# Optimization experiments

Hardware: AMD Instinct MI355X
Metric: run time of the kernel (lower is better)

The kernel has to match this reference:

```python
import jax, jax.numpy as jnp
import numpy as np

B, T, D, C = 8, 4096, 768, 2048

def setup_inputs() -> dict:
    key = jax.random.key(0)
    k1, k2 = jax.random.split(key)
    embed = jax.random.normal(k1, (B, T, D), dtype=jnp.float32)
    cluster_centers = jax.random.normal(k2, (C, D), dtype=jnp.float32)
    return {"embed": embed, "cluster_centers": cluster_centers}

def reference(embed, cluster_centers):
    x_sq = jnp.sum(embed * embed, axis=-1, keepdims=True)          # (b, t, 1)
    c_sq = jnp.sum(cluster_centers * cluster_centers, axis=-1)     # (c,)
    cross = jnp.einsum('btd,cd->btc', embed, cluster_centers)      # (b, t, c)
    sq_dists = x_sq + c_sq[None, None, :] - 2.0 * cross
    dists = jnp.sqrt(jnp.maximum(sq_dists, 0.0))
    # dists argmax of -cdist == argmin of cdist
    clusters = jnp.argmin(dists, axis=-1)                          # (b, t) int
    return clusters
```

## Files before the change

### kernel.cpp

```cpp
#include <hip/hip_runtime.h>

typedef __fp16 f16x2 __attribute__((ext_vector_type(2)));
typedef __fp16 f16x8 __attribute__((ext_vector_type(8)));
typedef float f32x4 __attribute__((ext_vector_type(4)));

constexpr int MM = 32768;
constexpr int NN = 2048;
constexpr int KK = 768;
constexpr int NKT = KK / 32;
constexpr int NA_UNITS = (MM / 16) * NKT;
constexpr int NB_UNITS = (NN / 16) * NKT;

constexpr size_t WS_APACK = 0;
constexpr size_t WS_BPACK = WS_APACK + (size_t)MM * KK * 4;
constexpr size_t WS_CSQ   = WS_BPACK + (size_t)NN * KK * 4;
constexpr size_t WS_SLOT  = WS_CSQ + (size_t)NN * 4;
constexpr size_t WS_NEED  = WS_SLOT + (size_t)MM * 16 * 8;

__device__ __forceinline__ unsigned bc(f16x2 h) {
    return __builtin_bit_cast(unsigned, h);
}


__global__ __launch_bounds__(256)
void fragpack_kernel(const float* __restrict__ A, const float* __restrict__ Bc,
                     uint4* __restrict__ Ap, uint4* __restrict__ Bp,
                     float* __restrict__ csq) {
    const int task = blockIdx.x * 4 + (threadIdx.x >> 6);
    const int lane = threadIdx.x & 63;

    if (task >= NA_UNITS + NB_UNITS) {
        const int cl = task - (NA_UNITS + NB_UNITS);
        const float4* row = reinterpret_cast<const float4*>(Bc + (size_t)cl * KK);
        float s = 0.f;
#pragma unroll
        for (int w = 0; w < KK / (4 * 64); ++w) {
            float4 v = row[w * 64 + lane];
            s = fmaf(v.x, v.x, s); s = fmaf(v.y, v.y, s);
            s = fmaf(v.z, v.z, s); s = fmaf(v.w, v.w, s);
        }
#pragma unroll
        for (int off = 32; off > 0; off >>= 1) s += __shfl_xor(s, off, 64);
        if (lane == 0) csq[cl] = s;
        return;
    }

    const int ln15 = lane & 15;
    const int quad = lane >> 4;

    const bool isB = task >= NA_UNITS;
    const int t = isB ? task - NA_UNITS : task;
    const int tile = t / NKT, kt = t % NKT;
    const float* src = (isB ? Bc : A) + (size_t)(tile * 16 + ln15) * KK + kt * 32 + quad * 8;
    uint4* dst = (isB ? Bp : Ap) + (size_t)t * 128 + lane;

    const float4 v0 = *(const float4*)(src);
    const float4 v1 = *(const float4*)(src + 4);
    f16x2 h0 = __builtin_amdgcn_cvt_pkrtz(v0.x, v0.y);
    f16x2 h1 = __builtin_amdgcn_cvt_pkrtz(v0.z, v0.w);
    f16x2 h2 = __builtin_amdgcn_cvt_pkrtz(v1.x, v1.y);
    f16x2 h3 = __builtin_amdgcn_cvt_pkrtz(v1.z, v1.w);
    f16x2 l0 = __builtin_amdgcn_cvt_pkrtz(v0.x-(float)h0[0], v0.y-(float)h0[1]);
    f16x2 l1 = __builtin_amdgcn_cvt_pkrtz(v0.z-(float)h1[0], v0.w-(float)h1[1]);
    f16x2 l2 = __builtin_amdgcn_cvt_pkrtz(v1.x-(float)h2[0], v1.y-(float)h2[1]);
    f16x2 l3 = __builtin_amdgcn_cvt_pkrtz(v1.z-(float)h3[0], v1.w-(float)h3[1]);
    uint4 hv = {bc(h0), bc(h1), bc(h2), bc(h3)};
    uint4 lv = {bc(l0), bc(l1), bc(l2), bc(l3)};
    dst[0]  = hv;
    dst[64] = lv;
}

__global__ __launch_bounds__(64)
void csq_kernel(const float* __restrict__ cc, float* __restrict__ csq) {
    const int cl = blockIdx.x;
    const int lane = threadIdx.x;
    const float4* row = reinterpret_cast<const float4*>(cc + (size_t)cl * KK);
    float s = 0.f;
#pragma unroll
    for (int w = 0; w < KK / (4 * 64); ++w) {
        float4 v = row[w * 64 + lane];
        s = fmaf(v.x, v.x, s); s = fmaf(v.y, v.y, s);
        s = fmaf(v.z, v.z, s); s = fmaf(v.w, v.w, s);
    }
#pragma unroll
    for (int off = 32; off > 0; off >>= 1) s += __shfl_xor(s, off, 64);
    if (lane == 0) csq[cl] = s;
}

#define MF2(a, b, c) __builtin_amdgcn_mfma_f32_16x16x32_f16(a, b, c, 0, 0, 0)
#define DSB() __builtin_amdgcn_sched_barrier(0)

__global__ __launch_bounds__(256, 3)
void gemm_pack_kernel(const uint4* __restrict__ Ap, const uint4* __restrict__ Bp,
                      const float* __restrict__ csq, uint2* __restrict__ slots) {
    __shared__ uint4 ldsq[2048];

    const int b   = blockIdx.x;
    const int xcd = b & 7;
    const int s   = b >> 3;
    const int gx  = s & 15;
    const int gy  = xcd + ((s >> 4) << 3);

    const int tid  = threadIdx.x;
    const int lane = tid & 63;
    const int ln15 = lane & 15;
    const int quad = lane >> 4;
    const int wave = tid >> 6;
    const int wm   = wave >> 1;
    const int wn   = wave & 1;
    const int tbase = gy * 128;
    const int cb    = gx * 128;

    const uint4* sp[8];
#pragma unroll
    for (int q = 0; q < 8; ++q) {
        const int u = wave * 8 + q;
        const bool isA = u < 16;
        const int v = isA ? u : u - 16;
        const int tile = (isA ? gy * 8 : gx * 8) + (v >> 1);
        const int part = v & 1;
        sp[q] = (isA ? Ap : Bp) + (size_t)tile * NKT * 128 + part * 64 + lane;
    }

#define STAGE_ALL(kt_) { if ((kt_) < NKT) {                                   \
    _Pragma("unroll")                                                         \
    for (int qq = 0; qq < 8; ++qq)                                            \
        __builtin_amdgcn_global_load_lds(                                     \
            (const __attribute__((address_space(1))) unsigned int*)(sp[qq] + (kt_) * 128), \
            (__attribute__((address_space(3))) unsigned int*)&ldsq[(wave * 8 + qq) * 64], \
            16, 0, 0); } }

    f32x4 acc[4][4];
#pragma unroll
    for (int i = 0; i < 4; ++i)
#pragma unroll
        for (int j = 0; j < 4; ++j) { f32x4 z = {0.f,0.f,0.f,0.f}; acc[i][j] = z; }

    f16x8 Bh[4], Bl[4], Ah[4], Al[4];

#define RD_ALL() {                                                            \
    _Pragma("unroll")                                                         \
    for (int j = 0; j < 4; ++j) {                                             \
        const int nu = 16 + (wn * 4 + j) * 2;                                 \
        Bh[j] = *(const f16x8*)&ldsq[nu * 64 + lane];                         \
        Bl[j] = *(const f16x8*)&ldsq[(nu + 1) * 64 + lane];                   \
    }                                                                         \
    _Pragma("unroll")                                                         \
    for (int i = 0; i < 4; ++i) {                                             \
        const int au = (wm * 4 + i) * 2;                                      \
        Ah[i] = *(const f16x8*)&ldsq[au * 64 + lane];                         \
        Al[i] = *(const f16x8*)&ldsq[(au + 1) * 64 + lane];                   \
    } }

#define MFMA_I2(i_) {                                                         \
    _Pragma("unroll")                                                         \
    for (int j = 0; j < 4; ++j) acc[i_][j] = MF2(Ah[i_], Bh[j], acc[i_][j]);  \
    _Pragma("unroll")                                                         \
    for (int j = 0; j < 4; ++j) acc[i_][j] = MF2(Ah[i_], Bl[j], acc[i_][j]);  \
    _Pragma("unroll")                                                         \
    for (int j = 0; j < 4; ++j) acc[i_][j] = MF2(Al[i_], Bh[j], acc[i_][j]);  \
}

#define WAIT_VM0()   { asm volatile("s_waitcnt vmcnt(0)" ::: "memory"); DSB(); }
#define WAIT_LGKM0() { asm volatile("s_waitcnt lgkmcnt(0)" ::: "memory"); DSB(); }
#define BARRIER()    { DSB(); __builtin_amdgcn_s_barrier(); DSB(); }

    STAGE_ALL(0)
    WAIT_VM0(); BARRIER();

#pragma unroll 1
    for (int kt = 0; kt < NKT; ++kt) {
        RD_ALL()
        MFMA_I2(0)
        WAIT_LGKM0();
        BARRIER();
        STAGE_ALL(kt + 1)
        DSB();
        MFMA_I2(1)
        MFMA_I2(2)
        MFMA_I2(3)
        WAIT_VM0();
        BARRIER();
    }

    float csq4[4];
#pragma unroll
    for (int j = 0; j < 4; ++j) csq4[j] = csq[cb + wn * 64 + j * 16 + ln15];

    float bval[16]; int bidx[16];
#pragma unroll
    for (int i = 0; i < 4; ++i)
#pragma unroll
        for (int r = 0; r < 4; ++r) {
            const int rid = i * 4 + r;
            float bv_ = csq4[0] - 2.0f * acc[i][0][r];
            int   bi_ = cb + wn * 64 + ln15;
#pragma unroll
            for (int j = 1; j < 4; ++j) {
                const float s2 = csq4[j] - 2.0f * acc[i][j][r];
                const int   c = cb + wn * 64 + j * 16 + ln15;
                if (s2 < bv_) { bv_ = s2; bi_ = c; }
            }
            bval[rid] = bv_; bidx[rid] = bi_;
        }
#pragma unroll
    for (int off = 1; off < 16; off <<= 1) {
#pragma unroll
        for (int rid = 0; rid < 16; ++rid) {
            const float ov = __shfl_xor(bval[rid], off, 64);
            const int   oi = __shfl_xor(bidx[rid], off, 64);
            if (ov < bval[rid] || (ov == bval[rid] && oi < bidx[rid])) {
                bval[rid] = ov; bidx[rid] = oi;
            }
        }
    }

    __syncthreads();
    float* vtab = (float*)&ldsq[0];
    int*   itab = (int*)&ldsq[64];
    if (ln15 == 0) {
#pragma unroll
        for (int i = 0; i < 4; ++i)
#pragma unroll
            for (int r = 0; r < 4; ++r) {
                const int row = wm * 64 + i * 16 + quad * 4 + r;
                vtab[row * 2 + wn] = bval[i * 4 + r];
                itab[row * 2 + wn] = bidx[i * 4 + r];
            }
    }
    __syncthreads();
    if (tid < 128) {
        float v0 = vtab[tid * 2]; int i0 = itab[tid * 2];
        const float v1 = vtab[tid * 2 + 1]; const int i1 = itab[tid * 2 + 1];
        if (v1 < v0 || (v1 == v0 && i1 < i0)) { v0 = v1; i0 = i1; }
        uint2 e; e.x = __float_as_uint(v0); e.y = (unsigned)i0;
        slots[(size_t)(tbase + tid) * 16 + gx] = e;
    }
}

__global__ __launch_bounds__(256)
void slot_reduce_kernel(const uint2* __restrict__ slots, int* __restrict__ out) {
    const int t = blockIdx.x * 256 + threadIdx.x;
    const uint2* s = slots + (size_t)t * 16;
    float bv = __uint_as_float(s[0].x); int bi = (int)s[0].y;
#pragma unroll
    for (int j = 1; j < 16; ++j) {
        const uint2 e = s[j];
        const float v = __uint_as_float(e.x);
        if (v < bv || (v == bv && (int)e.y < bi)) { bv = v; bi = (int)e.y; }
    }
    out[t] = bi;
}


__global__ __launch_bounds__(256)
void init_ws_kernel(unsigned long long* __restrict__ w) {
    w[blockIdx.x * 256 + threadIdx.x] = 0xFFFFFFFFFFFFFFFFull;
}

__global__ __launch_bounds__(256, 2)
void argmin_mfma_kernel(const float* __restrict__ A, const float* __restrict__ Bc,
                        const float* __restrict__ csq,
                        unsigned long long* __restrict__ ws64) {
    __shared__ unsigned lds[4 * 128 * 20];
    constexpr int AH = 0, AL = 2560, BH = 5120;

    const int tid  = threadIdx.x;
    const int lane = tid & 63;
    const int ln15 = lane & 15;
    const int quad = lane >> 4;
    const int wave = tid >> 6;
    const int wm = wave >> 1, wn = wave & 1;
    const int tbase = blockIdx.x * 128;
    const int cb    = blockIdx.y * 128;

    const int sr  = tid >> 1;
    const int skh = tid & 1;
    const float* gA = A  + (size_t)(tbase + sr) * KK + skh * 16;
    const float* gB = Bc + (size_t)(cb   + sr) * KK + skh * 16;
    const int wword = sr * 20 + skh * 8;

    f32x4 acc[4][4];
#pragma unroll
    for (int i = 0; i < 4; ++i)
#pragma unroll
        for (int j = 0; j < 4; ++j) { f32x4 z = {0.f,0.f,0.f,0.f}; acc[i][j] = z; }

    float4 av[4], bv[4];
#pragma unroll
    for (int p = 0; p < 4; ++p) {
        av[p] = *(const float4*)(gA + p * 4);
        bv[p] = *(const float4*)(gB + p * 4);
    }

    int aw[4], bw[4];
#pragma unroll
    for (int i = 0; i < 4; ++i) {
        aw[i] = AH + (wm * 64 + i * 16 + ln15) * 20 + quad * 4;
        bw[i] = BH + (wn * 64 + i * 16 + ln15) * 20 + quad * 4;
    }

    for (int k0 = 0; k0 < KK; k0 += 32) {
        __syncthreads();
#pragma unroll
        for (int h = 0; h < 2; ++h) {
            float4 v0 = av[2*h], v1 = av[2*h+1];
            f16x2 h00 = __builtin_amdgcn_cvt_pkrtz(v0.x, v0.y);
            f16x2 h01 = __builtin_amdgcn_cvt_pkrtz(v0.z, v0.w);
            f16x2 h10 = __builtin_amdgcn_cvt_pkrtz(v1.x, v1.y);
            f16x2 h11 = __builtin_amdgcn_cvt_pkrtz(v1.z, v1.w);
            f16x2 l00 = __builtin_amdgcn_cvt_pkrtz(v0.x-(float)h00[0], v0.y-(float)h00[1]);
            f16x2 l01 = __builtin_amdgcn_cvt_pkrtz(v0.z-(float)h01[0], v0.w-(float)h01[1]);
            f16x2 l10 = __builtin_amdgcn_cvt_pkrtz(v1.x-(float)h10[0], v1.y-(float)h10[1]);
            f16x2 l11 = __builtin_amdgcn_cvt_pkrtz(v1.z-(float)h11[0], v1.w-(float)h11[1]);
            uint4 hv = {bc(h00), bc(h01), bc(h10), bc(h11)};
            uint4 lv = {bc(l00), bc(l01), bc(l10), bc(l11)};
            *(uint4*)&lds[AH + wword + 4*h] = hv;
            *(uint4*)&lds[AL + wword + 4*h] = lv;

            float4 w0 = bv[2*h], w1 = bv[2*h+1];
            f16x2 g00 = __builtin_amdgcn_cvt_pkrtz(w0.x, w0.y);
            f16x2 g01 = __builtin_amdgcn_cvt_pkrtz(w0.z, w0.w);
            f16x2 g10 = __builtin_amdgcn_cvt_pkrtz(w1.x, w1.y);
            f16x2 g11 = __builtin_amdgcn_cvt_pkrtz(w1.z, w1.w);
            f16x2 m00 = __builtin_amdgcn_cvt_pkrtz(w0.x-(float)g00[0], w0.y-(float)g00[1]);
            f16x2 m01 = __builtin_amdgcn_cvt_pkrtz(w0.z-(float)g01[0], w0.w-(float)g01[1]);
            f16x2 m10 = __builtin_amdgcn_cvt_pkrtz(w1.x-(float)g10[0], w1.y-(float)g10[1]);
            f16x2 m11 = __builtin_amdgcn_cvt_pkrtz(w1.z-(float)g11[0], w1.w-(float)g11[1]);
            uint4 gv = {bc(g00), bc(g01), bc(g10), bc(g11)};
            uint4 mv = {bc(m00), bc(m01), bc(m10), bc(m11)};
            *(uint4*)&lds[BH + wword + 4*h]        = gv;
            *(uint4*)&lds[BH + 2560 + wword + 4*h] = mv;
        }
        __syncthreads();

        const int kn = k0 + 32;
        if (kn < KK) {
#pragma unroll
            for (int p = 0; p < 4; ++p) {
                av[p] = *(const float4*)(gA + kn + p * 4);
                bv[p] = *(const float4*)(gB + kn + p * 4);
            }
        }

        f16x8 a_h[4], a_l[4], b_h[4], b_l[4];
#pragma unroll
        for (int i = 0; i < 4; ++i) {
            a_h[i] = *(const f16x8*)&lds[aw[i]];
            a_l[i] = *(const f16x8*)&lds[aw[i] + 2560];
            b_h[i] = *(const f16x8*)&lds[bw[i]];
            b_l[i] = *(const f16x8*)&lds[bw[i] + 2560];
        }
#pragma unroll
        for (int i = 0; i < 4; ++i)
#pragma unroll
            for (int j = 0; j < 4; ++j) {
                acc[i][j] = __builtin_amdgcn_mfma_f32_16x16x32_f16(a_h[i], b_h[j], acc[i][j], 0, 0, 0);
                acc[i][j] = __builtin_amdgcn_mfma_f32_16x16x32_f16(a_h[i], b_l[j], acc[i][j], 0, 0, 0);
                acc[i][j] = __builtin_amdgcn_mfma_f32_16x16x32_f16(a_l[i], b_h[j], acc[i][j], 0, 0, 0);
            }
    }

    float csq4[4];
#pragma unroll
    for (int j = 0; j < 4; ++j) csq4[j] = csq[cb + wn * 64 + j * 16 + ln15];

    float bval[16]; int bidx[16];
#pragma unroll
    for (int i = 0; i < 4; ++i)
#pragma unroll
        for (int r = 0; r < 4; ++r) {
            const int rid = i * 4 + r;
            float bv_ = csq4[0] - 2.0f * acc[i][0][r];
            int   bi_ = cb + wn * 64 + ln15;
#pragma unroll
            for (int j = 1; j < 4; ++j) {
                const float s = csq4[j] - 2.0f * acc[i][j][r];
                const int   c = cb + wn * 64 + j * 16 + ln15;
                if (s < bv_) { bv_ = s; bi_ = c; }
            }
            bval[rid] = bv_; bidx[rid] = bi_;
        }
#pragma unroll
    for (int off = 1; off < 16; off <<= 1) {
#pragma unroll
        for (int rid = 0; rid < 16; ++rid) {
            const float ov = __shfl_xor(bval[rid], off, 64);
            const int   oi = __shfl_xor(bidx[rid], off, 64);
            if (ov < bval[rid] || (ov == bval[rid] && oi < bidx[rid])) {
                bval[rid] = ov; bidx[rid] = oi;
            }
        }
    }

    __syncthreads();
    float* vtab = (float*)&lds[0];
    int*   itab = (int*)&lds[256];
    if (ln15 == 0) {
#pragma unroll
        for (int i = 0; i < 4; ++i)
#pragma unroll
            for (int r = 0; r < 4; ++r) {
                const int row = wm * 64 + i * 16 + quad * 4 + r;
                vtab[row * 2 + wn] = bval[i * 4 + r];
                itab[row * 2 + wn] = bidx[i * 4 + r];
            }
    }
    __syncthreads();
    if (tid < 128) {
        float v0 = vtab[tid * 2]; int i0 = itab[tid * 2];
        const float v1 = vtab[tid * 2 + 1]; const int i1 = itab[tid * 2 + 1];
        if (v1 < v0 || (v1 == v0 && i1 < i0)) { v0 = v1; i0 = i1; }
        const unsigned b   = __float_as_uint(v0);
        const unsigned key = (b & 0x80000000u) ? ~b : (b | 0x80000000u);
        const unsigned long long pk =
            ((unsigned long long)key << 32) | (unsigned long long)(unsigned)i0;
        atomicMin(&ws64[tbase + tid], pk);
    }
}

__global__ __launch_bounds__(256)
void unpack_kernel(const unsigned long long* __restrict__ w, int* __restrict__ out) {
    const int i = blockIdx.x * 256 + threadIdx.x;
    out[i] = (int)(unsigned)(w[i] & 0xFFFFFFFFull);
}

extern "C" void kernel_launch(void* const* d_in, const int* in_sizes, int n_in,
                              void* d_out, int out_size, void* d_ws, size_t ws_size,
                              hipStream_t stream) {
    const float* embed   = (const float*)d_in[0];
    const float* centers = (const float*)d_in[1];
    int* out = (int*)d_out;

    if (ws_size >= WS_NEED) {
        uint4* Ap = (uint4*)((char*)d_ws + WS_APACK);
        uint4* Bp = (uint4*)((char*)d_ws + WS_BPACK);
        float* csq   = (float*)((char*)d_ws + WS_CSQ);
        uint2* slots = (uint2*)((char*)d_ws + WS_SLOT);
        fragpack_kernel<<<(NA_UNITS + NB_UNITS + NN) / 4, 256, 0, stream>>>(
            embed, centers, Ap, Bp, csq);
        gemm_pack_kernel<<<(MM / 128) * (NN / 128), 256, 0, stream>>>(
            Ap, Bp, csq, slots);
        slot_reduce_kernel<<<MM / 256, 256, 0, stream>>>(slots, out);
    } else {
        unsigned long long* ws64 = (unsigned long long*)d_ws;
        float* csq = (float*)((char*)d_ws + (size_t)MM * 8);
        init_ws_kernel<<<MM / 256, 256, 0, stream>>>(ws64);
        csq_kernel<<<NN, 64, 0, stream>>>(centers, csq);
        argmin_mfma_kernel<<<dim3(MM / 128, NN / 128), 256, 0, stream>>>(
            embed, centers, csq, ws64);
        unpack_kernel<<<MM / 256, 256, 0, stream>>>(ws64, out);
    }
}
```

Baseline: 435.4 us.

## Switch split-fp16 GEMM from 16x16x32 to 32x32x16 MFMA tiles

Repacks A and B fragments into 32-row by 16-k units and rewrites the GEMM inner loop to use 32x32x16 f16 MFMA with 2x2 accumulator tiles per wave instead of 4x4 16x16 tiles. The larger MFMA cuts the instruction count and LDS fragment reads per k-step. The argmin epilogue is rewritten for the 32x32 accumulator layout, with a 5-step shuffle reduction across 32 lanes. This risks different register pressure and epilogue shuffle cost.

```diff
diff --git a/kernel.cpp b/kernel.cpp
--- a/kernel.cpp
+++ b/kernel.cpp
@@ -3,13 +3,15 @@
 typedef __fp16 f16x2 __attribute__((ext_vector_type(2)));
 typedef __fp16 f16x8 __attribute__((ext_vector_type(8)));
 typedef float f32x4 __attribute__((ext_vector_type(4)));
+typedef float f32x16 __attribute__((ext_vector_type(16)));
 
 constexpr int MM = 32768;
 constexpr int NN = 2048;
 constexpr int KK = 768;
 constexpr int NKT = KK / 32;
-constexpr int NA_UNITS = (MM / 16) * NKT;
-constexpr int NB_UNITS = (NN / 16) * NKT;
+constexpr int NKT16 = KK / 16;
+constexpr int NA_UNITS = (MM / 32) * NKT16;
+constexpr int NB_UNITS = (NN / 32) * NKT16;
 
 constexpr size_t WS_APACK = 0;
 constexpr size_t WS_BPACK = WS_APACK + (size_t)MM * KK * 4;
@@ -45,13 +47,13 @@
         return;
     }
 
-    const int ln15 = lane & 15;
-    const int quad = lane >> 4;
+    const int ln31 = lane & 31;
+    const int half = lane >> 5;
 
     const bool isB = task >= NA_UNITS;
     const int t = isB ? task - NA_UNITS : task;
-    const int tile = t / NKT, kt = t % NKT;
-    const float* src = (isB ? Bc : A) + (size_t)(tile * 16 + ln15) * KK + kt * 32 + quad * 8;
+    const int tile = t / NKT16, kt = t % NKT16;
+    const float* src = (isB ? Bc : A) + (size_t)(tile * 32 + ln31) * KK + kt * 16 + half * 8;
     uint4* dst = (isB ? Bp : Ap) + (size_t)t * 128 + lane;
 
     const float4 v0 = *(const float4*)(src);
@@ -87,7 +89,7 @@
     if (lane == 0) csq[cl] = s;
 }
 
-#define MF2(a, b, c) __builtin_amdgcn_mfma_f32_16x16x32_f16(a, b, c, 0, 0, 0)
+#define MF32(a, b, c) __builtin_amdgcn_mfma_f32_32x32x16_f16(a, b, c, 0, 0, 0)
 #define DSB() __builtin_amdgcn_sched_barrier(0)
 
 __global__ __launch_bounds__(256, 3)
@@ -103,8 +105,8 @@
 
     const int tid  = threadIdx.x;
     const int lane = tid & 63;
-    const int ln15 = lane & 15;
-    const int quad = lane >> 4;
+    const int ln31 = lane & 31;
+    const int hi   = lane >> 5;
     const int wave = tid >> 6;
     const int wm   = wave >> 1;
     const int wn   = wave & 1;
@@ -116,49 +118,67 @@
     for (int q = 0; q < 8; ++q) {
         const int u = wave * 8 + q;
         const bool isA = u < 16;
-        const int v = isA ? u : u - 16;
-        const int tile = (isA ? gy * 8 : gx * 8) + (v >> 1);
+        const int v = u & 15;
+        const int tile = (isA ? gy * 4 : gx * 4) + (v >> 2);
+        const int ksub = (v >> 1) & 1;
         const int part = v & 1;
-        sp[q] = (isA ? Ap : Bp) + (size_t)tile * NKT * 128 + part * 64 + lane;
+        sp[q] = (isA ? Ap : Bp) + (size_t)(tile * NKT16 + ksub) * 128 + part * 64 + lane;
     }
 
 #define STAGE_ALL(kt_) { if ((kt_) < NKT) {                                   \
     _Pragma("unroll")                                                         \
     for (int qq = 0; qq < 8; ++qq)                                            \
         __builtin_amdgcn_global_load_lds(                                     \
-            (const __attribute__((address_space(1))) unsigned int*)(sp[qq] + (kt_) * 128), \
+            (const __attribute__((address_space(1))) unsigned int*)(sp[qq] + (kt_) * 256), \
             (__attribute__((address_space(3))) unsigned int*)&ldsq[(wave * 8 + qq) * 64], \
             16, 0, 0); } }
 
-    f32x4 acc[4][4];
-#pragma unroll
-    for (int i = 0; i < 4; ++i)
-#pragma unroll
-        for (int j = 0; j < 4; ++j) { f32x4 z = {0.f,0.f,0.f,0.f}; acc[i][j] = z; }
-
-    f16x8 Bh[4], Bl[4], Ah[4], Al[4];
+    f32x16 acc[2][2];
+#pragma unroll
+    for (int i = 0; i < 2; ++i)
+#pragma unroll
+        for (int j = 0; j < 2; ++j)
+#pragma unroll
+            for (int r = 0; r < 16; ++r) acc[i][j][r] = 0.f;
+
+    f16x8 Ah[2][2], Al[2][2], Bh[2][2], Bl[2][2];
 
 #define RD_ALL() {                                                            \
     _Pragma("unroll")                                                         \
-    for (int j = 0; j < 4; ++j) {                                             \
-        const int nu = 16 + (wn * 4 + j) * 2;                                 \
-        Bh[j] = *(const f16x8*)&ldsq[nu * 64 + lane];                         \
-        Bl[j] = *(const f16x8*)&ldsq[(nu + 1) * 64 + lane];                   \
+    for (int nj = 0; nj < 2; ++nj) {                                          \
+        const int nt = wn * 2 + nj;                                           \
+        _Pragma("unroll")                                                     \
+        for (int ks = 0; ks < 2; ++ks) {                                      \
+            Bh[nj][ks] = *(const f16x8*)&ldsq[1024 + (nt * 4 + ks * 2) * 64 + lane];     \
+            Bl[nj][ks] = *(const f16x8*)&ldsq[1024 + (nt * 4 + ks * 2 + 1) * 64 + lane]; \
+        }                                                                     \
     }                                                                         \
     _Pragma("unroll")                                                         \
-    for (int i = 0; i < 4; ++i) {                                             \
-        const int au = (wm * 4 + i) * 2;                                      \
-        Ah[i] = *(const f16x8*)&ldsq[au * 64 + lane];                         \
-        Al[i] = *(const f16x8*)&ldsq[(au + 1) * 64 + lane];                   \
+    for (int mi = 0; mi < 2; ++mi) {                                          \
+        const int mt = wm * 2 + mi;                                           \
+        _Pragma("unroll")                                                     \
+        for (int ks = 0; ks < 2; ++ks) {                                      \
+            Ah[mi][ks] = *(const f16x8*)&ldsq[(mt * 4 + ks * 2) * 64 + lane];            \
+            Al[mi][ks] = *(const f16x8*)&ldsq[(mt * 4 + ks * 2 + 1) * 64 + lane];        \
+        }                                                                     \
     } }
 
-#define MFMA_I2(i_) {                                                         \
-    _Pragma("unroll")                                                         \
-    for (int j = 0; j < 4; ++j) acc[i_][j] = MF2(Ah[i_], Bh[j], acc[i_][j]);  \
-    _Pragma("unroll")                                                         \
-    for (int j = 0; j < 4; ++j) acc[i_][j] = MF2(Ah[i_], Bl[j], acc[i_][j]);  \
-    _Pragma("unroll")                                                         \
-    for (int j = 0; j < 4; ++j) acc[i_][j] = MF2(Al[i_], Bh[j], acc[i_][j]);  \
+#define MFMA_KS(ks_) {                                                        \
+    _Pragma("unroll")                                                         \
+    for (int mi = 0; mi < 2; ++mi)                                            \
+        _Pragma("unroll")                                                     \
+        for (int nj = 0; nj < 2; ++nj)                                        \
+            acc[mi][nj] = MF32(Ah[mi][ks_], Bh[nj][ks_], acc[mi][nj]);        \
+    _Pragma("unroll")                                                         \
+    for (int mi = 0; mi < 2; ++mi)                                            \
+        _Pragma("unroll")                                                     \
+        for (int nj = 0; nj < 2; ++nj)                                        \
+            acc[mi][nj] = MF32(Ah[mi][ks_], Bl[nj][ks_], acc[mi][nj]);        \
+    _Pragma("unroll")                                                         \
+    for (int mi = 0; mi < 2; ++mi)                                            \
+        _Pragma("unroll")                                                     \
+        for (int nj = 0; nj < 2; ++nj)                                        \
+            acc[mi][nj] = MF32(Al[mi][ks_], Bh[nj][ks_], acc[mi][nj]);        \
 }
 
 #define WAIT_VM0()   { asm volatile("s_waitcnt vmcnt(0)" ::: "memory"); DSB(); }
@@ -171,62 +191,54 @@
 #pragma unroll 1
     for (int kt = 0; kt < NKT; ++kt) {
         RD_ALL()
-        MFMA_I2(0)
+        MFMA_KS(0)
         WAIT_LGKM0();
         BARRIER();
         STAGE_ALL(kt + 1)
         DSB();
-        MFMA_I2(1)
-        MFMA_I2(2)
-        MFMA_I2(3)
+        MFMA_KS(1)
         WAIT_VM0();
         BARRIER();
     }
 
-    float csq4[4];
-#pragma unroll
-    for (int j = 0; j < 4; ++j) csq4[j] = csq[cb + wn * 64 + j * 16 + ln15];
-
-    float bval[16]; int bidx[16];
-#pragma unroll
-    for (int i = 0; i < 4; ++i)
-#pragma unroll
-        for (int r = 0; r < 4; ++r) {
-            const int rid = i * 4 + r;
-            float bv_ = csq4[0] - 2.0f * acc[i][0][r];
-            int   bi_ = cb + wn * 64 + ln15;
-#pragma unroll
-            for (int j = 1; j < 4; ++j) {
-                const float s2 = csq4[j] - 2.0f * acc[i][j][r];
-                const int   c = cb + wn * 64 + j * 16 + ln15;
-                if (s2 < bv_) { bv_ = s2; bi_ = c; }
-            }
-            bval[rid] = bv_; bidx[rid] = bi_;
-        }
-#pragma unroll
-    for (int off = 1; off < 16; off <<= 1) {
-#pragma unroll
-        for (int rid = 0; rid < 16; ++rid) {
-            const float ov = __shfl_xor(bval[rid], off, 64);
-            const int   oi = __shfl_xor(bidx[rid], off, 64);
-            if (ov < bval[rid] || (ov == bval[rid] && oi < bidx[rid])) {
-                bval[rid] = ov; bidx[rid] = oi;
-            }
-        }
-    }
+    float csq2[2];
+#pragma unroll
+    for (int nj = 0; nj < 2; ++nj) csq2[nj] = csq[cb + wn * 64 + nj * 32 + ln31];
 
     __syncthreads();
     float* vtab = (float*)&ldsq[0];
     int*   itab = (int*)&ldsq[64];
-    if (ln15 == 0) {
-#pragma unroll
-        for (int i = 0; i < 4; ++i)
-#pragma unroll
-            for (int r = 0; r < 4; ++r) {
-                const int row = wm * 64 + i * 16 + quad * 4 + r;
-                vtab[row * 2 + wn] = bval[i * 4 + r];
-                itab[row * 2 + wn] = bidx[i * 4 + r];
-            }
+
+#pragma unroll
+    for (int mi = 0; mi < 2; ++mi) {
+        float bval[16]; int bidx[16];
+#pragma unroll
+        for (int r = 0; r < 16; ++r) {
+            float bv_ = csq2[0] - 2.0f * acc[mi][0][r];
+            int   bi_ = cb + wn * 64 + ln31;
+            const float s2 = csq2[1] - 2.0f * acc[mi][1][r];
+            if (s2 < bv_) { bv_ = s2; bi_ = cb + wn * 64 + 32 + ln31; }
+            bval[r] = bv_; bidx[r] = bi_;
+        }
+#pragma unroll
+        for (int off = 1; off < 32; off <<= 1) {
+#pragma unroll
+            for (int r = 0; r < 16; ++r) {
+                const float ov = __shfl_xor(bval[r], off, 64);
+                const int   oi = __shfl_xor(bidx[r], off, 64);
+                if (ov < bval[r] || (ov == bval[r] && oi < bidx[r])) {
+                    bval[r] = ov; bidx[r] = oi;
+                }
+            }
+        }
+        if (ln31 == 0) {
+#pragma unroll
+            for (int r = 0; r < 16; ++r) {
+                const int row = wm * 64 + mi * 32 + (r & 3) + 8 * (r >> 2) + 4 * hi;
+                vtab[row * 2 + wn] = bval[r];
+                itab[row * 2 + wn] = bidx[r];
+            }
+        }
     }
     __syncthreads();
     if (tid < 128) {
@@ -257,6 +269,8 @@
 void init_ws_kernel(unsigned long long* __restrict__ w) {
     w[blockIdx.x * 256 + threadIdx.x] = 0xFFFFFFFFFFFFFFFFull;
 }
+
+typedef float f32x4b __attribute__((ext_vector_type(4)));
 
 __global__ __launch_bounds__(256, 2)
 void argmin_mfma_kernel(const float* __restrict__ A, const float* __restrict__ Bc,
@@ -280,11 +294,11 @@
     const float* gB = Bc + (size_t)(cb   + sr) * KK + skh * 16;
     const int wword = sr * 20 + skh * 8;
 
-    f32x4 acc[4][4];
+    f32x4b acc[4][4];
 #pragma unroll
     for (int i = 0; i < 4; ++i)
 #pragma unroll
-        for (int j = 0; j < 4; ++j) { f32x4 z = {0.f,0.f,0.f,0.f}; acc[i][j] = z; }
+        for (int j = 0; j < 4; ++j) { f32x4b z = {0.f,0.f,0.f,0.f}; acc[i][j] = z; }
 
     float4 av[4], bv[4];
 #pragma unroll
```

Result: slower. 495.7 us (+13.9%).

## Double-buffer LDS staging and software-pipeline fragment reads with MFMA

Applied to the files above, without the earlier changes.

The GEMM main loop now uses two LDS buffers, so the global-to-LDS load for the next k-tile is issued at the start of each iteration into the other buffer. That removes one barrier per iteration. A-fragment reads are interleaved with MFMA groups through partial lgkmcnt waits, and B fragments for the next tile are prefetched into alternating register sets. This doubles LDS use and raises register pressure, so launch bounds drop from 3 to 2 blocks per CU, which reduces occupancy.

```diff
diff --git a/kernel.cpp b/kernel.cpp
--- a/kernel.cpp
+++ b/kernel.cpp
@@ -90,10 +90,10 @@
 #define MF2(a, b, c) __builtin_amdgcn_mfma_f32_16x16x32_f16(a, b, c, 0, 0, 0)
 #define DSB() __builtin_amdgcn_sched_barrier(0)
 
-__global__ __launch_bounds__(256, 3)
+__global__ __launch_bounds__(256, 2)
 void gemm_pack_kernel(const uint4* __restrict__ Ap, const uint4* __restrict__ Bp,
                       const float* __restrict__ csq, uint2* __restrict__ slots) {
-    __shared__ uint4 ldsq[2048];
+    __shared__ uint4 ldsq[4096];
 
     const int b   = blockIdx.x;
     const int xcd = b & 7;
@@ -122,13 +122,13 @@
         sp[q] = (isA ? Ap : Bp) + (size_t)tile * NKT * 128 + part * 64 + lane;
     }
 
-#define STAGE_ALL(kt_) { if ((kt_) < NKT) {                                   \
+#define STAGE_ALL(kt_, bufq_) {                                               \
     _Pragma("unroll")                                                         \
     for (int qq = 0; qq < 8; ++qq)                                            \
         __builtin_amdgcn_global_load_lds(                                     \
             (const __attribute__((address_space(1))) unsigned int*)(sp[qq] + (kt_) * 128), \
-            (__attribute__((address_space(3))) unsigned int*)&ldsq[(wave * 8 + qq) * 64], \
-            16, 0, 0); } }
+            (__attribute__((address_space(3))) unsigned int*)&ldsq[(bufq_) + (wave * 8 + qq) * 64], \
+            16, 0, 0); }
 
     f32x4 acc[4][4];
 #pragma unroll
@@ -136,51 +136,63 @@
 #pragma unroll
         for (int j = 0; j < 4; ++j) { f32x4 z = {0.f,0.f,0.f,0.f}; acc[i][j] = z; }
 
-    f16x8 Bh[4], Bl[4], Ah[4], Al[4];
-
-#define RD_ALL() {                                                            \
+    f16x8 AhE, AlE, AhO, AlO;
+    f16x8 BhE[4], BlE[4], BhO[4], BlO[4];
+
+#define RD_B2(bufq_, Bh_, Bl_) {                                              \
     _Pragma("unroll")                                                         \
     for (int j = 0; j < 4; ++j) {                                             \
         const int nu = 16 + (wn * 4 + j) * 2;                                 \
-        Bh[j] = *(const f16x8*)&ldsq[nu * 64 + lane];                         \
-        Bl[j] = *(const f16x8*)&ldsq[(nu + 1) * 64 + lane];                   \
-    }                                                                         \
+        Bh_[j] = *(const f16x8*)&ldsq[(bufq_) + nu * 64 + lane];              \
+        Bl_[j] = *(const f16x8*)&ldsq[(bufq_) + (nu + 1) * 64 + lane];        \
+    } }
+
+#define RD_A1(bufq_, i_, Ah_, Al_) {                                          \
+    const int au_ = (wm * 4 + (i_)) * 2;                                      \
+    Ah_ = *(const f16x8*)&ldsq[(bufq_) + au_ * 64 + lane];                    \
+    Al_ = *(const f16x8*)&ldsq[(bufq_) + (au_ + 1) * 64 + lane]; }
+
+#define MFMA_P(i_, Ah_, Al_, Bh_, Bl_) {                                      \
     _Pragma("unroll")                                                         \
-    for (int i = 0; i < 4; ++i) {                                             \
-        const int au = (wm * 4 + i) * 2;                                      \
-        Ah[i] = *(const f16x8*)&ldsq[au * 64 + lane];                         \
-        Al[i] = *(const f16x8*)&ldsq[(au + 1) * 64 + lane];                   \
-    } }
-
-#define MFMA_I2(i_) {                                                         \
+    for (int j = 0; j < 4; ++j) acc[i_][j] = MF2(Ah_, Bh_[j], acc[i_][j]);    \
     _Pragma("unroll")                                                         \
-    for (int j = 0; j < 4; ++j) acc[i_][j] = MF2(Ah[i_], Bh[j], acc[i_][j]);  \
+    for (int j = 0; j < 4; ++j) acc[i_][j] = MF2(Ah_, Bl_[j], acc[i_][j]);    \
     _Pragma("unroll")                                                         \
-    for (int j = 0; j < 4; ++j) acc[i_][j] = MF2(Ah[i_], Bl[j], acc[i_][j]);  \
-    _Pragma("unroll")                                                         \
-    for (int j = 0; j < 4; ++j) acc[i_][j] = MF2(Al[i_], Bh[j], acc[i_][j]);  \
-}
-
+    for (int j = 0; j < 4; ++j) acc[i_][j] = MF2(Al_, Bh_[j], acc[i_][j]);    \
+}
+
+#define LGKM2()  { asm volatile("s_waitcnt lgkmcnt(2)"  ::: "memory"); }
+#define LGKM10() { asm volatile("s_waitcnt lgkmcnt(10)" ::: "memory"); }
+#define LGKM0()  { asm volatile("s_waitcnt lgkmcnt(0)"  ::: "memory"); }
 #define WAIT_VM0()   { asm volatile("s_waitcnt vmcnt(0)" ::: "memory"); DSB(); }
-#define WAIT_LGKM0() { asm volatile("s_waitcnt lgkmcnt(0)" ::: "memory"); DSB(); }
 #define BARRIER()    { DSB(); __builtin_amdgcn_s_barrier(); DSB(); }
 
-    STAGE_ALL(0)
+#define BODY(kt_, cur_, nxt_, BhC, BlC, BhN, BlN)                             \
+    if ((kt_) + 1 < NKT) STAGE_ALL((kt_) + 1, nxt_)                           \
+    DSB();                                                                    \
+    RD_A1(cur_, 1, AhO, AlO) DSB(); LGKM2(); DSB();                           \
+    MFMA_P(0, AhE, AlE, BhC, BlC) DSB();                                      \
+    RD_A1(cur_, 2, AhE, AlE) DSB(); LGKM2(); DSB();                           \
+    MFMA_P(1, AhO, AlO, BhC, BlC) DSB();                                      \
+    RD_A1(cur_, 3, AhO, AlO) DSB(); LGKM2(); DSB();                           \
+    MFMA_P(2, AhE, AlE, BhC, BlC) DSB();                                      \
+    WAIT_VM0(); BARRIER();                                                    \
+    if ((kt_) + 1 < NKT) {                                                    \
+        RD_B2(nxt_, BhN, BlN) RD_A1(nxt_, 0, AhE, AlE)                        \
+        DSB(); LGKM10(); DSB();                                               \
+    } else { LGKM0(); DSB(); }                                                \
+    MFMA_P(3, AhO, AlO, BhC, BlC)                                             \
+    DSB();
+
+    STAGE_ALL(0, 0)
     WAIT_VM0(); BARRIER();
+    RD_B2(0, BhE, BlE) RD_A1(0, 0, AhE, AlE)
+    DSB();
 
 #pragma unroll 1
-    for (int kt = 0; kt < NKT; ++kt) {
-        RD_ALL()
-        MFMA_I2(0)
-        WAIT_LGKM0();
-        BARRIER();
-        STAGE_ALL(kt + 1)
-        DSB();
-        MFMA_I2(1)
-        MFMA_I2(2)
-        MFMA_I2(3)
-        WAIT_VM0();
-        BARRIER();
+    for (int kt2 = 0; kt2 < NKT; kt2 += 2) {
+        BODY(kt2,     0,    2048, BhE, BlE, BhO, BlO)
+        BODY(kt2 + 1, 2048, 0,    BhO, BlO, BhE, BlE)
     }
 
     float csq4[4];
```

Result: no change. 430.6 us (-1.1%).
